# Kernel tuning notes

Measured on AMD Instinct MI355X. Metric: run time of the kernel, lower is better.

Reference implementation:

```python
import jax, jax.numpy as jnp
import numpy as np

B, T, DIM, H, BUCKET = 4, 4096, 1024, 16, 64
E = DIM // H          # head dim = 64
U = T // BUCKET       # number of buckets = 64
EPS = 1e-6


def setup_inputs() -> dict:
    key = jax.random.key(0)
    ks = jax.random.split(key, 5)
    scale = 1.0 / np.sqrt(DIM)
    return {
        "x": jax.random.normal(ks[0], (B, T, DIM), dtype=jnp.float32),
        "Wq": jax.random.normal(ks[1], (DIM, DIM), dtype=jnp.float32) * scale,
        "Wk": jax.random.normal(ks[2], (DIM, DIM), dtype=jnp.float32) * scale,
        "Wv": jax.random.normal(ks[3], (DIM, DIM), dtype=jnp.float32) * scale,
        "Wo": jax.random.normal(ks[4], (DIM, DIM), dtype=jnp.float32) * scale,
        "bo": jnp.zeros((DIM,), dtype=jnp.float32),
    }


def _causal_linear_attn(q, k, v):
    # q, k, v: [b, h, t, e]; psi(k) = elu(k) + 1; q softmaxed over feature dim
    q = jax.nn.softmax(q, axis=-1)
    k = jax.nn.elu(k) + 1.0
    bucket = lambda x: x.reshape(*x.shape[:-2], U, BUCKET, E)  # [b,h,u,n,e]
    b_q, b_k, b_v = bucket(q), bucket(k), bucket(v)
    # cumulative key sums per bucket: [b,h,u,d]
    b_k_cumsum = jnp.cumsum(b_k.sum(axis=-2), axis=2)
    # per-bucket context then cumulative over buckets: [b,h,u,d,e]
    context = jnp.einsum("bhund,bhune->bhude", b_k, b_v)
    context = jnp.cumsum(context, axis=2)
    context = context / (b_k_cumsum[..., None] + EPS)
    # shift by one bucket (blindspot): bucket u sees context through bucket u-1
    context = jnp.concatenate(
        [jnp.zeros_like(context[:, :, :1]), context[:, :, :-1]], axis=2
    )
    attn = jnp.einsum("bhund,bhude->bhune", b_q, context)
    return attn.reshape(q.shape)  # [b,h,t,e]


def reference(x, Wq, Wk, Wv, Wo, bo):
    b, t, _ = x.shape
    q = x @ Wq
    k = x @ Wk
    v = x @ Wv
    merge = lambda z: z.reshape(b, t, H, E).transpose(0, 2, 1, 3)  # [b,h,t,e]
    attn = _causal_linear_attn(merge(q), merge(k), merge(v))
    out = attn.transpose(0, 2, 1, 3).reshape(b, t, DIM)
    return out @ Wo + bo
```

## Files before the change

kernel.cpp:

```cpp
#include <hip/hip_runtime.h>


#define T_LEN 4096
#define DIMN  1024
#define NHEAD 16
#define NB    4
#define MROWS (NB * T_LEN)

typedef float f32x4 __attribute__((ext_vector_type(4)));
typedef short s16x8 __attribute__((ext_vector_type(8)));
typedef short s16x4 __attribute__((ext_vector_type(4)));
using u16 = unsigned short;

__device__ __forceinline__ u16 f2bf(float f) {
  unsigned int u = __float_as_uint(f);
  u += 0x7fffu + ((u >> 16) & 1u);
  return (u16)(u >> 16);
}
__device__ __forceinline__ float bf2f(u16 h) {
  return __uint_as_float(((unsigned int)h) << 16);
}
__device__ __forceinline__ int swz16k(int off) {
  return off ^ (((off >> 7) & 3) << 4);
}

__global__ __launch_bounds__(256) void cvt_all_kern(const float* __restrict__ x,
                                                    const float* __restrict__ W0,
                                                    const float* __restrict__ W1,
                                                    const float* __restrict__ W2,
                                                    const float* __restrict__ W3,
                                                    u16* __restrict__ WT,
                                                    u16* __restrict__ xb) {
  __shared__ float tile[64][65];
  const int tid = threadIdx.x;
  if (blockIdx.x < 1024) {
    const int blk = blockIdx.x & 255;
    const int sel = blockIdx.x >> 8;
    const float* W = (sel == 0) ? W0 : (sel == 1) ? W1 : (sel == 2) ? W2 : W3;
    u16* dst = WT + (size_t)sel * DIMN * DIMN;
    const int k0 = (blk >> 4) << 6;
    const int n0 = (blk & 15) << 6;
    const int r = tid >> 6;
    const int c = tid & 63;
#pragma unroll
    for (int i = 0; i < 16; ++i) {
      int row = (i << 2) + r;
      tile[row][c] = W[(size_t)(k0 + row) * DIMN + n0 + c];
    }
    __syncthreads();
#pragma unroll
    for (int i = 0; i < 16; ++i) {
      int row = (i << 2) + r;
      dst[(size_t)(n0 + row) * DIMN + k0 + c] = f2bf(tile[c][row]);
    }
  } else {
    size_t i = ((size_t)(blockIdx.x - 1024) * 256 + tid) * 4;
    f32x4 v = *(const f32x4*)(x + i);
    s16x4 o;
    o.x = (short)f2bf(v.x); o.y = (short)f2bf(v.y);
    o.z = (short)f2bf(v.z); o.w = (short)f2bf(v.w);
    *(s16x4*)(xb + i) = o;
  }
}

template <int MODE>
__global__ __launch_bounds__(512, 4) void gemm_t(
    const u16* __restrict__ A, const u16* __restrict__ Bt,
    u16* __restrict__ dq, u16* __restrict__ dk, u16* __restrict__ dv,
    float* __restrict__ dO, const float* __restrict__ bias) {
  constexpr int K = 1024;
  constexpr int BNT = (MODE == 0) ? 12 : 4;
  constexpr int NT = K / 32;
  __shared__ char lds[49152];

  const int tid = threadIdx.x;
  const int l = tid & 63;
  const int w = tid >> 6;
  const int wm = w >> 2;
  const int wn = w & 3;

  const int xcd = (int)blockIdx.x & 7;
  const int idx = (int)blockIdx.x >> 3;
  const int g = idx / (4 * BNT);
  const int r2 = idx % (4 * BNT);
  const int bn = r2 >> 2;
  const int bm = xcd * 16 + g * 4 + (r2 & 3);
  const size_t arow0 = (size_t)bm * 128;
  const size_t brow0 = (size_t)bn * 256;

  int lrow[2], lcol[2];
#pragma unroll
  for (int i = 0; i < 2; ++i) {
    int lg = swz16k(tid * 16 + i * 8192);
    lrow[i] = lg >> 6;
    lcol[i] = (lg & 63) >> 1;
  }

  const int fr = l & 15;
  const int kswz = (((l >> 4) << 4)) ^ ((((fr >> 1) & 3)) << 4);

  auto STAGE = [&](int matsel, int tt) {
    const int kbase = (tt & (NT - 1)) * 32;
#pragma unroll
    for (int i = 0; i < 2; ++i) {
      if (matsel == 0 && i == 1) break;
      const u16* src = (matsel == 0)
          ? A  + (arow0 + (size_t)lrow[i]) * K + kbase + lcol[i]
          : Bt + (brow0 + (size_t)lrow[i]) * K + kbase + lcol[i];
      char* dst = lds + ((tt & 1) * 24576 + matsel * 8192 + i * 8192 + tid * 16);
      __builtin_amdgcn_global_load_lds(
          (__attribute__((address_space(1))) const void*)src,
          (__attribute__((address_space(3))) void*)dst, 16, 0, 0);
    }
  };
  auto LDA = [&](int buf, int rowb) -> s16x8 {
    return *(const s16x8*)(lds + buf * 24576 + rowb * 64 + kswz);
  };
  auto LDB = [&](int buf, int rowb) -> s16x8 {
    return *(const s16x8*)(lds + buf * 24576 + 8192 + rowb * 64 + kswz);
  };

  f32x4 acc[4][4];
#pragma unroll
  for (int i = 0; i < 4; ++i)
#pragma unroll
    for (int j = 0; j < 4; ++j) acc[i][j] = {0.f, 0.f, 0.f, 0.f};

  STAGE(0, 0); STAGE(1, 0);
  asm volatile("s_waitcnt vmcnt(0)" ::: "memory");
  __builtin_amdgcn_sched_barrier(0);
  __builtin_amdgcn_s_barrier();

  const int amb = wm * 64;
  const int bnb = wn * 64;
  s16x8 af[4], bf[4];

#define STEP(BUF, T)                                                          \
  {                                                                           \
    STAGE(0, (T) + 1);                                                        \
    STAGE(1, (T) + 1);                                                        \
    _Pragma("unroll")                                                         \
    for (int i = 0; i < 4; ++i) af[i] = LDA((BUF), amb + i * 16 + fr);        \
    _Pragma("unroll")                                                         \
    for (int i = 0; i < 4; ++i) bf[i] = LDB((BUF), bnb + i * 16 + fr);        \
    __builtin_amdgcn_s_setprio(1);                                            \
    _Pragma("unroll")                                                         \
    for (int mi = 0; mi < 4; ++mi)                                            \
      _Pragma("unroll")                                                       \
      for (int ni = 0; ni < 4; ++ni)                                          \
        acc[mi][ni] = __builtin_amdgcn_mfma_f32_16x16x32_bf16(                \
            af[mi], bf[ni], acc[mi][ni], 0, 0, 0);                            \
    __builtin_amdgcn_s_setprio(0);                                            \
    asm volatile("s_waitcnt vmcnt(0)" ::: "memory");                          \
    __builtin_amdgcn_sched_barrier(0);                                        \
    __builtin_amdgcn_s_barrier();                                             \
  }

#pragma unroll 1
  for (int th = 0; th < NT / 2; ++th) {
    STEP(0, 2 * th)
    STEP(1, 2 * th + 1)
  }
#undef STEP

  const int r0 = (l >> 4) << 2;
  const int c0 = l & 15;
  if constexpr (MODE == 0) {
    const int mat = bn >> 2;
    u16* dst = (mat == 0) ? dq : ((mat == 1) ? dk : dv);
    const size_t colbase = (size_t)(bn & 3) * 256 + (size_t)wn * 64;
    if (mat == 0) {
#pragma unroll
      for (int mi = 0; mi < 4; ++mi) {
#pragma unroll
        for (int j = 0; j < 4; ++j) {
          float v0 = acc[mi][0][j], v1 = acc[mi][1][j];
          float v2 = acc[mi][2][j], v3 = acc[mi][3][j];
          float m = fmaxf(fmaxf(v0, v1), fmaxf(v2, v3));
#pragma unroll
          for (int off = 1; off < 16; off <<= 1) m = fmaxf(m, __shfl_xor(m, off));
          float e0 = __expf(v0 - m), e1 = __expf(v1 - m);
          float e2 = __expf(v2 - m), e3 = __expf(v3 - m);
          float s = e0 + e1 + e2 + e3;
#pragma unroll
          for (int off = 1; off < 16; off <<= 1) s += __shfl_xor(s, off);
          float inv = 1.f / s;
          const size_t row = arow0 + wm * 64 + mi * 16 + r0 + j;
          u16* p = dst + row * DIMN + colbase + c0;
          p[0]  = f2bf(e0 * inv); p[16] = f2bf(e1 * inv);
          p[32] = f2bf(e2 * inv); p[48] = f2bf(e3 * inv);
        }
      }
    } else {
#pragma unroll
      for (int mi = 0; mi < 4; ++mi)
#pragma unroll
        for (int ni = 0; ni < 4; ++ni)
#pragma unroll
          for (int j = 0; j < 4; ++j) {
            const size_t row = arow0 + wm * 64 + mi * 16 + r0 + j;
            float v = acc[mi][ni][j];
            float r = (mat == 1) ? (v > 0.f ? v + 1.f : __expf(v)) : v;
            dst[row * DIMN + colbase + ni * 16 + c0] = f2bf(r);
          }
    }
  } else {
#pragma unroll
    for (int mi = 0; mi < 4; ++mi)
#pragma unroll
      for (int ni = 0; ni < 4; ++ni) {
        const size_t col = brow0 + (size_t)wn * 64 + ni * 16 + c0;
        const float bv = bias[col];
#pragma unroll
        for (int j = 0; j < 4; ++j) {
          const size_t row = arow0 + wm * 64 + mi * 16 + r0 + j;
          dO[row * DIMN + col] = acc[mi][ni][j] + bv;
        }
      }
  }
}

__global__ __launch_bounds__(256) void ctx_bucket_kern(const u16* __restrict__ kb,
                                                       const u16* __restrict__ vb,
                                                       u16* __restrict__ ctx,
                                                       float* __restrict__ ksum) {
  __shared__ float kl[4096];
  __shared__ float vl[4096];
  const int blk = blockIdx.x;
  const int u = blk & 63;
  const int bh = blk >> 6;
  const int b = bh >> 4, h = bh & 15;
  const size_t rowbase = (size_t)b * T_LEN + (size_t)u * 64;
  const int tid = threadIdx.x;
#pragma unroll
  for (int i = 0; i < 16; ++i) {
    int idx = i * 256 + tid;
    int n = idx >> 6, d = idx & 63;
    size_t g = (rowbase + n) * DIMN + (size_t)h * 64 + d;
    kl[idx] = bf2f(kb[g]);
    vl[idx] = bf2f(vb[g]);
  }
  __syncthreads();
  const int dq = (tid & 15) << 2;
  const int eq = (tid >> 4) << 2;
  float a[4][4] = {};
  float ks[4] = {};
  for (int n = 0; n < 64; ++n) {
    f32x4 kv = *(const f32x4*)&kl[n * 64 + dq];
    f32x4 vv = *(const f32x4*)&vl[n * 64 + eq];
#pragma unroll
    for (int i = 0; i < 4; ++i) {
      ks[i] += kv[i];
#pragma unroll
      for (int j = 0; j < 4; ++j) a[i][j] += kv[i] * vv[j];
    }
  }
  const size_t cbase = (size_t)blk * 4096;
#pragma unroll
  for (int i = 0; i < 4; ++i) {
    s16x4 o;
    o.x = (short)f2bf(a[i][0]); o.y = (short)f2bf(a[i][1]);
    o.z = (short)f2bf(a[i][2]); o.w = (short)f2bf(a[i][3]);
    *(s16x4*)&ctx[cbase + (size_t)(dq + i) * 64 + eq] = o;
  }
  if ((tid >> 4) == 0) {
    f32x4 o = {ks[0], ks[1], ks[2], ks[3]};
    *(f32x4*)&ksum[(size_t)blk * 64 + dq] = o;
  }
}

__global__ __launch_bounds__(256) void ctx_cumnorm_kern(u16* __restrict__ ctx,
                                                        const float* __restrict__ ksum) {
  const int tid = blockIdx.x * 256 + threadIdx.x;
  const int bh = tid >> 10;
  const int rem = tid & 1023;
  const int d = rem >> 4;
  const int e0 = (rem & 15) << 2;
  float c0 = 0.f, c1 = 0.f, c2 = 0.f, c3 = 0.f, accK = 0.f;
  for (int u = 0; u < 64; ++u) {
    const size_t base = ((size_t)(bh * 64 + u)) * 4096 + (size_t)d * 64 + e0;
    s16x4 cv4 = *(const s16x4*)&ctx[base];
    float kk = ksum[(size_t)(bh * 64 + u) * 64 + d];
    float x0 = bf2f((u16)cv4.x), x1 = bf2f((u16)cv4.y);
    float x2 = bf2f((u16)cv4.z), x3 = bf2f((u16)cv4.w);
    s16x4 o;
    if (u == 0) {
      o.x = 0; o.y = 0; o.z = 0; o.w = 0;
    } else {
      float inv = 1.f / (accK + 1e-6f);
      o.x = (short)f2bf(c0 * inv); o.y = (short)f2bf(c1 * inv);
      o.z = (short)f2bf(c2 * inv); o.w = (short)f2bf(c3 * inv);
    }
    *(s16x4*)&ctx[base] = o;
    c0 += x0; c1 += x1; c2 += x2; c3 += x3;
    accK += kk;
  }
}

__global__ __launch_bounds__(256) void attn_bucket_kern(const u16* __restrict__ qb,
                                                        const u16* __restrict__ ctx,
                                                        u16* __restrict__ attn) {
  __shared__ float qT[64 * 68];
  __shared__ float cl[4096];
  const int blk = blockIdx.x;
  const int u = blk & 63;
  const int bh = blk >> 6;
  const int b = bh >> 4, h = bh & 15;
  const size_t rowbase = (size_t)b * T_LEN + (size_t)u * 64;
  const int tid = threadIdx.x;
  const size_t cbase = (size_t)blk * 4096;
#pragma unroll
  for (int i = 0; i < 16; ++i) {
    int idx = i * 256 + tid;
    int n = idx >> 6, d = idx & 63;
    qT[d * 68 + n] = bf2f(qb[(rowbase + n) * DIMN + (size_t)h * 64 + d]);
  }
#pragma unroll
  for (int i = 0; i < 4; ++i) {
    int idx4 = (i * 256 + tid) * 4;
    s16x4 cv = *(const s16x4*)&ctx[cbase + idx4];
    cl[idx4]     = bf2f((u16)cv.x);
    cl[idx4 + 1] = bf2f((u16)cv.y);
    cl[idx4 + 2] = bf2f((u16)cv.z);
    cl[idx4 + 3] = bf2f((u16)cv.w);
  }
  __syncthreads();
  const int nq = (tid & 15) << 2;
  const int eq = (tid >> 4) << 2;
  float a[4][4] = {};
  for (int d = 0; d < 64; ++d) {
    f32x4 qv = *(const f32x4*)&qT[d * 68 + nq];
    f32x4 cv = *(const f32x4*)&cl[d * 64 + eq];
#pragma unroll
    for (int i = 0; i < 4; ++i)
#pragma unroll
      for (int j = 0; j < 4; ++j) a[i][j] += qv[i] * cv[j];
  }
#pragma unroll
  for (int i = 0; i < 4; ++i) {
    s16x4 o;
    o.x = (short)f2bf(a[i][0]); o.y = (short)f2bf(a[i][1]);
    o.z = (short)f2bf(a[i][2]); o.w = (short)f2bf(a[i][3]);
    *(s16x4*)&attn[(rowbase + nq + i) * DIMN + (size_t)h * 64 + eq] = o;
  }
}

extern "C" void kernel_launch(void* const* d_in, const int* in_sizes, int n_in,
                              void* d_out, int out_size, void* d_ws, size_t ws_size,
                              hipStream_t stream) {
  const float* x  = (const float*)d_in[0];
  const float* Wq = (const float*)d_in[1];
  const float* Wk = (const float*)d_in[2];
  const float* Wv = (const float*)d_in[3];
  const float* Wo = (const float*)d_in[4];
  const float* bo = (const float*)d_in[5];
  float* out = (float*)d_out;

  constexpr size_t SZ_XB = (size_t)MROWS * DIMN * 2;
  constexpr size_t SZ_WT = (size_t)DIMN * DIMN * 2;
  constexpr size_t SZ_CTX = (size_t)NB * NHEAD * 64 * 64 * 64 * 2;
  char* ws = (char*)d_ws;
  u16*   xb   = (u16*)(ws);
  u16*   wqT  = (u16*)(ws + SZ_XB);
  u16*   woT  = (u16*)(ws + SZ_XB + 3 * SZ_WT);
  u16*   qb   = (u16*)(ws + SZ_XB + 4 * SZ_WT);
  u16*   kb   = (u16*)(ws + 2 * SZ_XB + 4 * SZ_WT);
  u16*   vb   = (u16*)(ws + 3 * SZ_XB + 4 * SZ_WT);
  u16*   ctx  = (u16*)(ws + 4 * SZ_XB + 4 * SZ_WT);
  float* ksum = (float*)(ws + 4 * SZ_XB + 4 * SZ_WT + SZ_CTX);
  u16*   attn = xb;

  cvt_all_kern<<<1024 + MROWS * DIMN / 1024, 256, 0, stream>>>(x, Wq, Wk, Wv, Wo,
                                                               wqT, xb);

  gemm_t<0><<<1536, 512, 0, stream>>>(xb, wqT, qb, kb, vb, nullptr, nullptr);

  ctx_bucket_kern<<<NB * NHEAD * 64, 256, 0, stream>>>(kb, vb, ctx, ksum);
  ctx_cumnorm_kern<<<256, 256, 0, stream>>>(ctx, ksum);
  attn_bucket_kern<<<NB * NHEAD * 64, 256, 0, stream>>>(qb, ctx, attn);

  gemm_t<1><<<512, 512, 0, stream>>>(attn, woT, nullptr, nullptr, nullptr, out, bo);
}
```

Baseline: 262.8 us.

## Enlarge GEMM tiles to 256x256 with K=64 stages and split-phase pipelining

Replaces the 128x256 GEMM tile with a 256x256 tile and a K-step of 64 held in 128KB of dynamic LDS, with double buffering. The K-tile is split into four MFMA phases, and each phase prefetches the next half-tile of A or B between barriers. The goal is to raise arithmetic intensity per staged byte and overlap global-to-LDS loads with MFMA work. The cost is more registers (32 accumulators per wave), lower occupancy (launch bounds 2), fewer blocks (768 and 256), and extra barriers per K-tile.

```diff
diff --git a/kernel.cpp b/kernel.cpp
--- a/kernel.cpp
+++ b/kernel.cpp
@@ -19,9 +19,6 @@
 }
 __device__ __forceinline__ float bf2f(u16 h) {
   return __uint_as_float(((unsigned int)h) << 16);
-}
-__device__ __forceinline__ int swz16k(int off) {
-  return off ^ (((off >> 7) & 3) << 4);
 }
 
 __global__ __launch_bounds__(256) void cvt_all_kern(const float* __restrict__ x,
@@ -64,14 +61,14 @@
 }
 
 template <int MODE>
-__global__ __launch_bounds__(512, 4) void gemm_t(
+__global__ __launch_bounds__(512, 2) void gemm256(
     const u16* __restrict__ A, const u16* __restrict__ Bt,
     u16* __restrict__ dq, u16* __restrict__ dk, u16* __restrict__ dv,
     float* __restrict__ dO, const float* __restrict__ bias) {
   constexpr int K = 1024;
   constexpr int BNT = (MODE == 0) ? 12 : 4;
-  constexpr int NT = K / 32;
-  __shared__ char lds[49152];
+  constexpr int NT = K / 64;
+  extern __shared__ char lds[];
 
   const int tid = threadIdx.x;
   const int l = tid & 63;
@@ -81,87 +78,132 @@
 
   const int xcd = (int)blockIdx.x & 7;
   const int idx = (int)blockIdx.x >> 3;
-  const int g = idx / (4 * BNT);
+  const int gg = idx / (4 * BNT);
   const int r2 = idx % (4 * BNT);
   const int bn = r2 >> 2;
-  const int bm = xcd * 16 + g * 4 + (r2 & 3);
-  const size_t arow0 = (size_t)bm * 128;
+  const int bm = xcd * 8 + gg * 4 + (r2 & 3);
+  const size_t arow0 = (size_t)bm * 256;
   const size_t brow0 = (size_t)bn * 256;
 
-  int lrow[2], lcol[2];
-#pragma unroll
-  for (int i = 0; i < 2; ++i) {
-    int lg = swz16k(tid * 16 + i * 8192);
-    lrow[i] = lg >> 6;
-    lcol[i] = (lg & 63) >> 1;
-  }
-
-  const int fr = l & 15;
-  const int kswz = (((l >> 4) << 4)) ^ ((((fr >> 1) & 3)) << 4);
-
-  auto STAGE = [&](int matsel, int tt) {
-    const int kbase = (tt & (NT - 1)) * 32;
+  const int srow0 = tid >> 3;
+  const int scol = (((tid & 7) ^ ((tid >> 3) & 7)) << 3);
+
+  auto STAGE = [&](int mat, int half, int tt) {
+    const int kbase = (tt & (NT - 1)) * 64;
 #pragma unroll
     for (int i = 0; i < 2; ++i) {
-      if (matsel == 0 && i == 1) break;
-      const u16* src = (matsel == 0)
-          ? A  + (arow0 + (size_t)lrow[i]) * K + kbase + lcol[i]
-          : Bt + (brow0 + (size_t)lrow[i]) * K + kbase + lcol[i];
-      char* dst = lds + ((tt & 1) * 24576 + matsel * 8192 + i * 8192 + tid * 16);
+      const size_t grow = (mat == 0 ? arow0 : brow0) + half * 128 + i * 64 + srow0;
+      const u16* src = (mat == 0 ? A : Bt) + grow * K + kbase + scol;
+      char* dst = lds + ((tt & 1) * 65536 + mat * 32768 + half * 16384 +
+                         i * 8192 + tid * 16);
       __builtin_amdgcn_global_load_lds(
           (__attribute__((address_space(1))) const void*)src,
           (__attribute__((address_space(3))) void*)dst, 16, 0, 0);
     }
   };
-  auto LDA = [&](int buf, int rowb) -> s16x8 {
-    return *(const s16x8*)(lds + buf * 24576 + rowb * 64 + kswz);
+
+  const int fr = l & 15;
+  const int kb16 = (l >> 4) << 4;
+  auto LDA = [&](int buf, int miH, int mi2, int kk) -> s16x8 {
+    const int lr = miH * 64 + mi2 * 16 + fr;
+    const int kByte = (kk * 64 + kb16) ^ ((lr & 7) << 4);
+    return *(const s16x8*)(lds + buf * 65536 + wm * 16384 + lr * 128 + kByte);
   };
-  auto LDB = [&](int buf, int rowb) -> s16x8 {
-    return *(const s16x8*)(lds + buf * 24576 + 8192 + rowb * 64 + kswz);
+  auto LDB = [&](int buf, int ni, int kk) -> s16x8 {
+    const int lr = (wn & 1) * 64 + ni * 16 + fr;
+    const int kByte = (kk * 64 + kb16) ^ ((lr & 7) << 4);
+    return *(const s16x8*)(lds + buf * 65536 + 32768 + (wn >> 1) * 16384 +
+                           lr * 128 + kByte);
   };
 
-  f32x4 acc[4][4];
-#pragma unroll
-  for (int i = 0; i < 4; ++i)
+  f32x4 acc[8][4];
+#pragma unroll
+  for (int i = 0; i < 8; ++i)
 #pragma unroll
     for (int j = 0; j < 4; ++j) acc[i][j] = {0.f, 0.f, 0.f, 0.f};
 
-  STAGE(0, 0); STAGE(1, 0);
+  STAGE(0, 0, 0); STAGE(0, 1, 0); STAGE(1, 0, 0); STAGE(1, 1, 0);
+  STAGE(0, 0, 1); STAGE(0, 1, 1);
+  asm volatile("s_waitcnt vmcnt(4)" ::: "memory");
+  __builtin_amdgcn_sched_barrier(0);
+  __builtin_amdgcn_s_barrier();
+
+  s16x8 a0q[4][2], a1q[4][2], b0q[2][2], b1q[2][2];
+
+#define MFMA16(AQ, NIOFF, BQ)                                                 \
+  __builtin_amdgcn_s_setprio(1);                                              \
+  _Pragma("unroll")                                                           \
+  for (int mi = 0; mi < 4; ++mi)                                              \
+    _Pragma("unroll")                                                         \
+    for (int ni = 0; ni < 2; ++ni)                                            \
+      _Pragma("unroll")                                                       \
+      for (int kk = 0; kk < 2; ++kk)                                          \
+        acc[(AQ##_OFF) + mi][(NIOFF) + ni] =                                  \
+            __builtin_amdgcn_mfma_f32_16x16x32_bf16(                          \
+                AQ[mi][kk], BQ[ni][kk], acc[(AQ##_OFF) + mi][(NIOFF) + ni],   \
+                0, 0, 0);                                                     \
+  __builtin_amdgcn_s_setprio(0);
+
+#define KTILE(BUF, T)                                                         \
+  {                                                                           \
+    enum { a0q_OFF = 0, a1q_OFF = 4 };                                        \
+                                                                 \
+    STAGE(1, 0, (T) + 1);                                                     \
+    _Pragma("unroll")                                                         \
+    for (int mi = 0; mi < 4; ++mi)                                            \
+      _Pragma("unroll")                                                       \
+      for (int kk = 0; kk < 2; ++kk) a0q[mi][kk] = LDA((BUF), 0, mi, kk);     \
+    _Pragma("unroll")                                                         \
+    for (int ni = 0; ni < 2; ++ni)                                            \
+      _Pragma("unroll")                                                       \
+      for (int kk = 0; kk < 2; ++kk) b0q[ni][kk] = LDB((BUF), ni, kk);        \
+    __builtin_amdgcn_s_barrier();                                             \
+    asm volatile("s_waitcnt lgkmcnt(0)" ::: "memory");                        \
+    __builtin_amdgcn_sched_barrier(0);                                        \
+    MFMA16(a0q, 0, b0q)                                                       \
+    __builtin_amdgcn_s_barrier();                                             \
+                                                                 \
+    STAGE(1, 1, (T) + 1);                                                     \
+    _Pragma("unroll")                                                         \
+    for (int mi = 0; mi < 4; ++mi)                                            \
+      _Pragma("unroll")                                                       \
+      for (int kk = 0; kk < 2; ++kk) a1q[mi][kk] = LDA((BUF), 1, mi, kk);     \
+    __builtin_amdgcn_s_barrier();                                             \
+    asm volatile("s_waitcnt lgkmcnt(0)" ::: "memory");                        \
+    __builtin_amdgcn_sched_barrier(0);                                        \
+    MFMA16(a1q, 0, b0q)                                                       \
+    __builtin_amdgcn_s_barrier();                                             \
+                                                                 \
+    STAGE(0, 0, (T) + 2);                                                     \
+    _Pragma("unroll")                                                         \
+    for (int ni = 0; ni < 2; ++ni)                                            \
+      _Pragma("unroll")                                                       \
+      for (int kk = 0; kk < 2; ++kk) b1q[ni][kk] = LDB((BUF), 2 + ni, kk);    \
+    __builtin_amdgcn_s_barrier();                                             \
+    asm volatile("s_waitcnt lgkmcnt(0)" ::: "memory");                        \
+    __builtin_amdgcn_sched_barrier(0);                                        \
+    MFMA16(a0q, 2, b1q)                                                       \
+    __builtin_amdgcn_s_barrier();                                             \
+                                                       \
+    STAGE(0, 1, (T) + 2);                                                     \
+    __builtin_amdgcn_s_barrier();                                             \
+    MFMA16(a1q, 2, b1q)                                                       \
+    asm volatile("s_waitcnt vmcnt(4)" ::: "memory");                          \
+    __builtin_amdgcn_sched_barrier(0);                                        \
+    __builtin_amdgcn_s_barrier();                                             \
+  }
+
+#pragma unroll 1
+  for (int th = 0; th < NT / 2; ++th) {
+    KTILE(0, 2 * th)
+    KTILE(1, 2 * th + 1)
+  }
+#undef KTILE
+#undef MFMA16
+
   asm volatile("s_waitcnt vmcnt(0)" ::: "memory");
   __builtin_amdgcn_sched_barrier(0);
   __builtin_amdgcn_s_barrier();
-
-  const int amb = wm * 64;
-  const int bnb = wn * 64;
-  s16x8 af[4], bf[4];
-
-#define STEP(BUF, T)                                                          \
-  {                                                                           \
-    STAGE(0, (T) + 1);                                                        \
-    STAGE(1, (T) + 1);                                                        \
-    _Pragma("unroll")                                                         \
-    for (int i = 0; i < 4; ++i) af[i] = LDA((BUF), amb + i * 16 + fr);        \
-    _Pragma("unroll")                                                         \
-    for (int i = 0; i < 4; ++i) bf[i] = LDB((BUF), bnb + i * 16 + fr);        \
-    __builtin_amdgcn_s_setprio(1);                                            \
-    _Pragma("unroll")                                                         \
-    for (int mi = 0; mi < 4; ++mi)                                            \
-      _Pragma("unroll")                                                       \
-      for (int ni = 0; ni < 4; ++ni)                                          \
-        acc[mi][ni] = __builtin_amdgcn_mfma_f32_16x16x32_bf16(                \
-            af[mi], bf[ni], acc[mi][ni], 0, 0, 0);                            \
-    __builtin_amdgcn_s_setprio(0);                                            \
-    asm volatile("s_waitcnt vmcnt(0)" ::: "memory");                          \
-    __builtin_amdgcn_sched_barrier(0);                                        \
-    __builtin_amdgcn_s_barrier();                                             \
-  }
-
-#pragma unroll 1
-  for (int th = 0; th < NT / 2; ++th) {
-    STEP(0, 2 * th)
-    STEP(1, 2 * th + 1)
-  }
-#undef STEP
 
   const int r0 = (l >> 4) << 2;
   const int c0 = l & 15;
@@ -171,11 +213,11 @@
     const size_t colbase = (size_t)(bn & 3) * 256 + (size_t)wn * 64;
     if (mat == 0) {
 #pragma unroll
-      for (int mi = 0; mi < 4; ++mi) {
+      for (int a = 0; a < 8; ++a) {
 #pragma unroll
         for (int j = 0; j < 4; ++j) {
-          float v0 = acc[mi][0][j], v1 = acc[mi][1][j];
-          float v2 = acc[mi][2][j], v3 = acc[mi][3][j];
+          float v0 = acc[a][0][j], v1 = acc[a][1][j];
+          float v2 = acc[a][2][j], v3 = acc[a][3][j];
           float m = fmaxf(fmaxf(v0, v1), fmaxf(v2, v3));
 #pragma unroll
           for (int off = 1; off < 16; off <<= 1) m = fmaxf(m, __shfl_xor(m, off));
@@ -185,7 +227,7 @@
 #pragma unroll
           for (int off = 1; off < 16; off <<= 1) s += __shfl_xor(s, off);
           float inv = 1.f / s;
-          const size_t row = arow0 + wm * 64 + mi * 16 + r0 + j;
+          const size_t row = arow0 + wm * 128 + (a >> 2) * 64 + (a & 3) * 16 + r0 + j;
           u16* p = dst + row * DIMN + colbase + c0;
           p[0]  = f2bf(e0 * inv); p[16] = f2bf(e1 * inv);
           p[32] = f2bf(e2 * inv); p[48] = f2bf(e3 * inv);
@@ -193,28 +235,28 @@
       }
     } else {
 #pragma unroll
-      for (int mi = 0; mi < 4; ++mi)
+      for (int a = 0; a < 8; ++a)
 #pragma unroll
         for (int ni = 0; ni < 4; ++ni)
 #pragma unroll
           for (int j = 0; j < 4; ++j) {
-            const size_t row = arow0 + wm * 64 + mi * 16 + r0 + j;
-            float v = acc[mi][ni][j];
+            const size_t row = arow0 + wm * 128 + (a >> 2) * 64 + (a & 3) * 16 + r0 + j;
+            float v = acc[a][ni][j];
             float r = (mat == 1) ? (v > 0.f ? v + 1.f : __expf(v)) : v;
             dst[row * DIMN + colbase + ni * 16 + c0] = f2bf(r);
           }
     }
   } else {
 #pragma unroll
-    for (int mi = 0; mi < 4; ++mi)
+    for (int a = 0; a < 8; ++a)
 #pragma unroll
       for (int ni = 0; ni < 4; ++ni) {
         const size_t col = brow0 + (size_t)wn * 64 + ni * 16 + c0;
         const float bv = bias[col];
 #pragma unroll
         for (int j = 0; j < 4; ++j) {
-          const size_t row = arow0 + wm * 64 + mi * 16 + r0 + j;
-          dO[row * DIMN + col] = acc[mi][ni][j] + bv;
+          const size_t row = arow0 + wm * 128 + (a >> 2) * 64 + (a & 3) * 16 + r0 + j;
+          dO[row * DIMN + col] = acc[a][ni][j] + bv;
         }
       }
   }
@@ -370,14 +412,19 @@
   float* ksum = (float*)(ws + 4 * SZ_XB + 4 * SZ_WT + SZ_CTX);
   u16*   attn = xb;
 
+  (void)hipFuncSetAttribute((const void*)gemm256<0>,
+                            hipFuncAttributeMaxDynamicSharedMemorySize, 131072);
+  (void)hipFuncSetAttribute((const void*)gemm256<1>,
+                            hipFuncAttributeMaxDynamicSharedMemorySize, 131072);
+
   cvt_all_kern<<<1024 + MROWS * DIMN / 1024, 256, 0, stream>>>(x, Wq, Wk, Wv, Wo,
                                                                wqT, xb);
 
-  gemm_t<0><<<1536, 512, 0, stream>>>(xb, wqT, qb, kb, vb, nullptr, nullptr);
+  gemm256<0><<<768, 512, 131072, stream>>>(xb, wqT, qb, kb, vb, nullptr, nullptr);
 
   ctx_bucket_kern<<<NB * NHEAD * 64, 256, 0, stream>>>(kb, vb, ctx, ksum);
   ctx_cumnorm_kern<<<256, 256, 0, stream>>>(ctx, ksum);
   attn_bucket_kern<<<NB * NHEAD * 64, 256, 0, stream>>>(qb, ctx, attn);
 
-  gemm_t<1><<<512, 512, 0, stream>>>(attn, woT, nullptr, nullptr, nullptr, out, bo);
-}
+  gemm256<1><<<256, 512, 131072, stream>>>(attn, woT, nullptr, nullptr, nullptr, out, bo);
+}
```

Result: no change. 259.1 us (-1.4%).

## Triple-buffer GEMM LDS staging to prefetch two K-tiles ahead

Applied to the files above, without the earlier changes.

Moves the bf16 GEMM main loop from double to triple LDS buffering. Global-to-LDS loads are now issued two K-steps ahead, and each step waits only for the older batch (vmcnt(3)) instead of draining all outstanding loads. The aim is to hide global memory latency behind the MFMA work. In exchange, LDS per block grows from 48 KB to 72 KB, which may cut the number of resident blocks below the launch-bounds target of 4 and so reduce occupancy. It also uses runtime buffer indices in place of compile-time constants.

```diff
diff --git a/kernel.cpp b/kernel.cpp
--- a/kernel.cpp
+++ b/kernel.cpp
@@ -71,7 +71,7 @@
   constexpr int K = 1024;
   constexpr int BNT = (MODE == 0) ? 12 : 4;
   constexpr int NT = K / 32;
-  __shared__ char lds[49152];
+  __shared__ char lds[73728];
 
   const int tid = threadIdx.x;
   const int l = tid & 63;
@@ -99,7 +99,7 @@
   const int fr = l & 15;
   const int kswz = (((l >> 4) << 4)) ^ ((((fr >> 1) & 3)) << 4);
 
-  auto STAGE = [&](int matsel, int tt) {
+  auto STAGE = [&](int buf, int matsel, int tt) {
     const int kbase = (tt & (NT - 1)) * 32;
 #pragma unroll
     for (int i = 0; i < 2; ++i) {
@@ -107,7 +107,7 @@
       const u16* src = (matsel == 0)
           ? A  + (arow0 + (size_t)lrow[i]) * K + kbase + lcol[i]
           : Bt + (brow0 + (size_t)lrow[i]) * K + kbase + lcol[i];
-      char* dst = lds + ((tt & 1) * 24576 + matsel * 8192 + i * 8192 + tid * 16);
+      char* dst = lds + (buf * 24576 + matsel * 8192 + i * 8192 + tid * 16);
       __builtin_amdgcn_global_load_lds(
           (__attribute__((address_space(1))) const void*)src,
           (__attribute__((address_space(3))) void*)dst, 16, 0, 0);
@@ -126,8 +126,9 @@
 #pragma unroll
     for (int j = 0; j < 4; ++j) acc[i][j] = {0.f, 0.f, 0.f, 0.f};
 
-  STAGE(0, 0); STAGE(1, 0);
-  asm volatile("s_waitcnt vmcnt(0)" ::: "memory");
+  STAGE(0, 0, 0); STAGE(0, 1, 0);
+  STAGE(1, 0, 1); STAGE(1, 1, 1);
+  asm volatile("s_waitcnt vmcnt(3)" ::: "memory");
   __builtin_amdgcn_sched_barrier(0);
   __builtin_amdgcn_s_barrier();
 
@@ -135,33 +136,29 @@
   const int bnb = wn * 64;
   s16x8 af[4], bf[4];
 
-#define STEP(BUF, T)                                                          \
-  {                                                                           \
-    STAGE(0, (T) + 1);                                                        \
-    STAGE(1, (T) + 1);                                                        \
-    _Pragma("unroll")                                                         \
-    for (int i = 0; i < 4; ++i) af[i] = LDA((BUF), amb + i * 16 + fr);        \
-    _Pragma("unroll")                                                         \
-    for (int i = 0; i < 4; ++i) bf[i] = LDB((BUF), bnb + i * 16 + fr);        \
-    __builtin_amdgcn_s_setprio(1);                                            \
-    _Pragma("unroll")                                                         \
-    for (int mi = 0; mi < 4; ++mi)                                            \
-      _Pragma("unroll")                                                       \
-      for (int ni = 0; ni < 4; ++ni)                                          \
-        acc[mi][ni] = __builtin_amdgcn_mfma_f32_16x16x32_bf16(                \
-            af[mi], bf[ni], acc[mi][ni], 0, 0, 0);                            \
-    __builtin_amdgcn_s_setprio(0);                                            \
-    asm volatile("s_waitcnt vmcnt(0)" ::: "memory");                          \
-    __builtin_amdgcn_sched_barrier(0);                                        \
-    __builtin_amdgcn_s_barrier();                                             \
-  }
-
+  int bufR = 0, bufW = 2;
 #pragma unroll 1
-  for (int th = 0; th < NT / 2; ++th) {
-    STEP(0, 2 * th)
-    STEP(1, 2 * th + 1)
-  }
-#undef STEP
+  for (int t = 0; t < NT; ++t) {
+    STAGE(bufW, 0, t + 2);
+    STAGE(bufW, 1, t + 2);
+#pragma unroll
+    for (int i = 0; i < 4; ++i) af[i] = LDA(bufR, amb + i * 16 + fr);
+#pragma unroll
+    for (int i = 0; i < 4; ++i) bf[i] = LDB(bufR, bnb + i * 16 + fr);
+    __builtin_amdgcn_s_setprio(1);
+#pragma unroll
+    for (int mi = 0; mi < 4; ++mi)
+#pragma unroll
+      for (int ni = 0; ni < 4; ++ni)
+        acc[mi][ni] = __builtin_amdgcn_mfma_f32_16x16x32_bf16(
+            af[mi], bf[ni], acc[mi][ni], 0, 0, 0);
+    __builtin_amdgcn_s_setprio(0);
+    asm volatile("s_waitcnt vmcnt(3)" ::: "memory");
+    __builtin_amdgcn_sched_barrier(0);
+    __builtin_amdgcn_s_barrier();
+    bufR = (bufR == 2) ? 0 : bufR + 1;
+    bufW = (bufW == 2) ? 0 : bufW + 1;
+  }
 
   const int r0 = (l >> 4) << 2;
   const int c0 = l & 15;
```

After: 268.2 us. 2.0% more time.
